# Kernel tuning notes

Hardware: AMD Instinct MI355X
Metric: run time of the kernel (lower is better)

## Reference

```python
import jax, jax.numpy as jnp
import numpy as np

B, H, S, DK = 4, 16, 2048, 128

def setup_inputs() -> dict:
    key = jax.random.key(0)
    kq, kk, kv, km = jax.random.split(key, 4)
    query = jax.random.normal(kq, (B, H, S, DK), dtype=jnp.float32)
    key_t = jax.random.normal(kk, (B, H, S, DK), dtype=jnp.float32)
    value = jax.random.normal(kv, (B, H, S, DK), dtype=jnp.float32)
    mask = jax.random.randint(km, (B, H, S, S), 0, 2, dtype=jnp.int32)
    return {"query": query, "key": key_t, "value": value, "mask": mask}

def reference(query, key, value, mask):
    d_k = query.shape[-1]
    # scores: (b, h, sq, sk)
    scores = jnp.einsum("bhqd,bhkd->bhqk", query, key) / jnp.sqrt(jnp.float32(d_k))
    scores = jnp.where(mask == 0, -jnp.inf, scores)
    weights = jax.nn.softmax(scores, axis=-1)  # dropout p=0.0 -> identity
    out = jnp.einsum("bhqk,bhkd->bhqd", weights, value)
    return out, weights
```

## Files before the change

### kernel.cpp

```cpp
#include <hip/hip_runtime.h>


constexpr int Sc = 2048, Dc = 128;
constexpr int BHc = 64;
constexpr long OUTE = (long)BHc * Sc * Dc;
constexpr long KVE  = (long)BHc * Sc * Dc;
constexpr int QBR = 128;
constexpr int NQT = Sc / QBR;
constexpr int NBLK = BHc * NQT;
#define SCALEF 0.088388347648318447f

typedef __attribute__((ext_vector_type(4))) float f32x4;
typedef _Float16 f16x8 __attribute__((ext_vector_type(8)));

static __device__ __forceinline__ f16x8 loadcvt8h(const float* __restrict__ p) {
  float4 a = *(const float4*)p;
  float4 b = *(const float4*)(p + 4);
  f16x8 r;
  r[0] = (_Float16)a.x; r[1] = (_Float16)a.y; r[2] = (_Float16)a.z; r[3] = (_Float16)a.w;
  r[4] = (_Float16)b.x; r[5] = (_Float16)b.y; r[6] = (_Float16)b.z; r[7] = (_Float16)b.w;
  return r;
}

__global__ __launch_bounds__(256)
void kconv_kernel(const float* __restrict__ K, _Float16* __restrict__ Kh) {
  long i = ((long)blockIdx.x * 256 + threadIdx.x) * 8;
  f16x8 v = loadcvt8h(K + i);
  *(f16x8*)(Kh + i) = v;
}

__global__ __launch_bounds__(256)
void vtrans_kernel(const float* __restrict__ V, _Float16* __restrict__ Vt) {
  __shared__ _Float16 sT[Dc][64 + 2];
  const int bh = blockIdx.x >> 5;
  const int kt = blockIdx.x & 31;
  const int tid = threadIdx.x;
  const float* vb = V + ((long)bh * Sc + kt * 64) * Dc;
  #pragma unroll
  for (int i = 0; i < 8; i++) {
    int e = tid + i * 256;
    int ki = e >> 5;
    int dq = (e & 31) * 4;
    float4 f = *(const float4*)(vb + (long)ki * Dc + dq);
    sT[dq + 0][ki] = (_Float16)f.x;
    sT[dq + 1][ki] = (_Float16)f.y;
    sT[dq + 2][ki] = (_Float16)f.z;
    sT[dq + 3][ki] = (_Float16)f.w;
  }
  __syncthreads();
  #pragma unroll
  for (int i = 0; i < 4; i++) {
    int chunk = tid + i * 256;
    int d = chunk >> 3;
    int kc = (chunk & 7) * 8;
    f16x8 o;
    #pragma unroll
    for (int j = 0; j < 8; j++) o[j] = sT[d][kc + j];
    *(f16x8*)(Vt + ((long)bh * Dc + d) * Sc + kt * 64 + kc) = o;
  }
}

__global__ __launch_bounds__(512, 4)
void sdpa_main(const float* __restrict__ Qg, const int* __restrict__ Mg,
               float* __restrict__ Og, const _Float16* __restrict__ Kh,
               const _Float16* __restrict__ Vt, unsigned* __restrict__ msk) {
  __shared__ __align__(16) _Float16 sKd[2][64][136];
  __shared__ __align__(16) _Float16 sV[128][72];
  __shared__ __align__(16) _Float16 sPw[8][16][76];
  __shared__ float sRinv[QBR];

  const int bid0 = blockIdx.x;
  const int bid  = (bid0 & 7) * (NBLK >> 3) + (bid0 >> 3);
  const int bh = bid >> 4;
  const int qt = bid & (NQT - 1);

  const int tid  = threadIdx.x;
  const int lane = tid & 63;
  const int w = tid >> 6;
  const int g = lane >> 4;
  const int c = lane & 15;

  f16x8 aq[4];
  {
    const float* qp = Qg + ((long)bh * Sc + (long)qt * QBR + w * 16 + c) * Dc + g * 8;
    #pragma unroll
    for (int ch = 0; ch < 4; ch++) aq[ch] = loadcvt8h(qp + ch * 32);
  }

  const _Float16* Kplane = Kh + (long)bh * Sc * Dc;
  const _Float16* Vplane = Vt + (long)bh * Dc * Sc;
  const int* Mwave = Mg + ((long)bh * Sc + (long)qt * QBR + w * 16 + g * 4) * Sc;
  unsigned* mskB = msk + (long)bid0 * (16 * 512);

  const int kr0 = tid >> 4, kd0 = tid & 15;
  const int vr0 = tid >> 3, vc0 = tid & 7;

  auto loadK = [&](int cc, f16x8& a, f16x8& b) {
    a = *(const f16x8*)(Kplane + (long)(cc * 64 + kr0) * Dc + kd0 * 8);
    b = *(const f16x8*)(Kplane + (long)(cc * 64 + kr0 + 32) * Dc + kd0 * 8);
  };
  auto stageK = [&](int p, const f16x8& a, const f16x8& b) {
    *(f16x8*)&sKd[p][kr0][kd0 * 8] = a;
    *(f16x8*)&sKd[p][kr0 + 32][kd0 * 8] = b;
  };
  auto loadV = [&](int cc, f16x8& a, f16x8& b) {
    a = *(const f16x8*)(Vplane + (long)vr0 * Sc + cc * 64 + vc0 * 8);
    b = *(const f16x8*)(Vplane + (long)(vr0 + 64) * Sc + cc * 64 + vc0 * 8);
  };
  auto stageV = [&](const f16x8& a, const f16x8& b) {
    *(f16x8*)&sV[vr0][vc0 * 8] = a;
    *(f16x8*)&sV[vr0 + 64][vc0 * 8] = b;
  };
  auto loadM = [&](int (*dst)[4], int cc) {
    const int* mp = Mwave + cc * 64 + c;
    #pragma unroll
    for (int nt = 0; nt < 4; nt++)
      #pragma unroll
      for (int r = 0; r < 4; r++)
        dst[nt][r] = mp[(long)r * Sc + nt * 16];
  };
  auto packbits = [&](const int (*mv)[4]) -> unsigned {
    unsigned bits = 0;
    #pragma unroll
    for (int nt = 0; nt < 4; nt++)
      #pragma unroll
      for (int r = 0; r < 4; r++)
        bits |= (mv[nt][r] != 0 ? 1u : 0u) << (nt * 4 + r);
    return bits;
  };

  auto qkTile = [&](int p, int nt) -> f32x4 {
    const _Float16* kb = &sKd[p][nt * 16 + c][g * 8];
    f16x8 b0 = *(const f16x8*)kb;
    f16x8 b1 = *(const f16x8*)(kb + 32);
    f16x8 b2 = *(const f16x8*)(kb + 64);
    f16x8 b3 = *(const f16x8*)(kb + 96);
    f32x4 s = {0.f, 0.f, 0.f, 0.f};
    s = __builtin_amdgcn_mfma_f32_16x16x32_f16(aq[0], b0, s, 0, 0, 0);
    s = __builtin_amdgcn_mfma_f32_16x16x32_f16(aq[1], b1, s, 0, 0, 0);
    s = __builtin_amdgcn_mfma_f32_16x16x32_f16(aq[2], b2, s, 0, 0, 0);
    s = __builtin_amdgcn_mfma_f32_16x16x32_f16(aq[3], b3, s, 0, 0, 0);
    return s;
  };

  float rs[4] = {0.f, 0.f, 0.f, 0.f};
  {
    f16x8 ka0, kb0, ka1, kb1;
    int mv0[4][4], mv1[4][4];
    auto bodyA = [&](int p, unsigned bits) {
      #pragma unroll
      for (int nt = 0; nt < 4; nt++) {
        f32x4 s = qkTile(p, nt);
        #pragma unroll
        for (int r = 0; r < 4; r++) {
          float e = ((bits >> (nt * 4 + r)) & 1u) ? __expf(s[r] * SCALEF) : 0.f;
          rs[r] += (float)(_Float16)e;
        }
      }
    };
    loadK(0, ka0, kb0);
    loadM(mv0, 0);
    for (int cc = 0; cc < 32; cc += 2) {
      stageK(0, ka0, kb0);
      __syncthreads();
      loadK(cc + 1, ka1, kb1);
      loadM(mv1, cc + 1);
      const unsigned bits0 = packbits(mv0);
      bodyA(0, bits0);
      stageK(1, ka1, kb1);
      __syncthreads();
      if (cc + 2 < 32) {
        loadK(cc + 2, ka0, kb0);
        loadM(mv0, cc + 2);
      }
      const unsigned bits1 = packbits(mv1);
      mskB[((cc >> 1) << 9) + tid] = bits0 | (bits1 << 16);
      bodyA(1, bits1);
    }
  }
  #pragma unroll
  for (int r = 0; r < 4; r++) {
    float x = rs[r];
    x += __shfl_xor(x, 1);
    x += __shfl_xor(x, 2);
    x += __shfl_xor(x, 4);
    x += __shfl_xor(x, 8);
    if (c == 0) sRinv[w * 16 + g * 4 + r] = (x > 0.f) ? (1.f / x) : 0.f;
  }
  __syncthreads();
  const float rinvW = sRinv[w * 16 + (lane >> 2)];
  float rinvO[4];
  #pragma unroll
  for (int r = 0; r < 4; r++) rinvO[r] = sRinv[w * 16 + g * 4 + r];

  f32x4 oacc[8];
  #pragma unroll
  for (int dt = 0; dt < 8; dt++) oacc[dt] = (f32x4){0.f, 0.f, 0.f, 0.f};
  float* wbase = Og + OUTE + ((long)bh * Sc + (long)qt * QBR + w * 16) * Sc;
  const int wr = lane >> 2;
  const int wq = lane & 3;

  {
    f16x8 ka, kb2, va, vb2;
    loadK(0, ka, kb2);
    loadV(0, va, vb2);
    unsigned bp = mskB[tid];
    unsigned bpn = 0;
    for (int cc = 0; cc < 32; cc++) {
      __syncthreads();
      stageK(0, ka, kb2);
      stageV(va, vb2);
      __syncthreads();
      if (cc + 1 < 32) {
        loadK(cc + 1, ka, kb2);
        loadV(cc + 1, va, vb2);
      }
      if ((cc & 1) == 0 && (cc >> 1) + 1 < 16)
        bpn = mskB[(((cc >> 1) + 1) << 9) + tid];
      const unsigned bits = (cc & 1) ? (bp >> 16) : (bp & 0xffffu);
      #pragma unroll
      for (int nt = 0; nt < 4; nt++) {
        f32x4 s = qkTile(0, nt);
        #pragma unroll
        for (int r = 0; r < 4; r++) {
          float e = ((bits >> (nt * 4 + r)) & 1u) ? __expf(s[r] * SCALEF) : 0.f;
          sPw[w][g * 4 + r][nt * 16 + c] = (_Float16)e;
        }
      }
      {
        f16x8 p0 = *(const f16x8*)&sPw[w][wr][wq * 16];
        f16x8 p1 = *(const f16x8*)&sPw[w][wr][wq * 16 + 8];
        float* dst = wbase + (long)wr * Sc + cc * 64 + wq * 16;
        float4 o0, o1, o2, o3;
        o0.x = (float)p0[0] * rinvW; o0.y = (float)p0[1] * rinvW;
        o0.z = (float)p0[2] * rinvW; o0.w = (float)p0[3] * rinvW;
        o1.x = (float)p0[4] * rinvW; o1.y = (float)p0[5] * rinvW;
        o1.z = (float)p0[6] * rinvW; o1.w = (float)p0[7] * rinvW;
        o2.x = (float)p1[0] * rinvW; o2.y = (float)p1[1] * rinvW;
        o2.z = (float)p1[2] * rinvW; o2.w = (float)p1[3] * rinvW;
        o3.x = (float)p1[4] * rinvW; o3.y = (float)p1[5] * rinvW;
        o3.z = (float)p1[6] * rinvW; o3.w = (float)p1[7] * rinvW;
        *(float4*)dst = o0;
        *(float4*)(dst + 4) = o1;
        *(float4*)(dst + 8) = o2;
        *(float4*)(dst + 12) = o3;
      }
      f16x8 pa0 = *(const f16x8*)&sPw[w][c][g * 8];
      f16x8 pa1 = *(const f16x8*)&sPw[w][c][32 + g * 8];
      #pragma unroll
      for (int dt = 0; dt < 8; dt++) {
        const _Float16* vb = &sV[dt * 16 + c][g * 8];
        f16x8 v0 = *(const f16x8*)vb;
        f16x8 v1 = *(const f16x8*)(vb + 32);
        oacc[dt] = __builtin_amdgcn_mfma_f32_16x16x32_f16(pa0, v0, oacc[dt], 0, 0, 0);
        oacc[dt] = __builtin_amdgcn_mfma_f32_16x16x32_f16(pa1, v1, oacc[dt], 0, 0, 0);
      }
      if (cc & 1) bp = bpn;
    }
  }

  float* ob = Og + ((long)bh * Sc + (long)qt * QBR + w * 16 + g * 4) * Dc;
  #pragma unroll
  for (int r = 0; r < 4; r++) {
    #pragma unroll
    for (int dt = 0; dt < 8; dt++) {
      ob[(long)r * Dc + dt * 16 + c] = oacc[dt][r] * rinvO[r];
    }
  }
}

__global__ __launch_bounds__(256)
void sdpa_naive(const float* __restrict__ Qg, const float* __restrict__ Kg,
                const float* __restrict__ Vg, const int* __restrict__ Mg,
                float* __restrict__ Og) {
  __shared__ float sE[4][Sc];
  const int bh = blockIdx.x >> 9;
  const int rg = blockIdx.x & 511;
  const int wv = threadIdx.x >> 6, ln = threadIdx.x & 63;
  const int qrow = rg * 4 + wv;
  const float* qp = Qg + ((long)bh * Sc + qrow) * Dc;
  const int* mp = Mg + ((long)bh * Sc + qrow) * Sc;
  float rsum = 0.f;
  for (int k0 = 0; k0 < Sc; k0 += 64) {
    const int kcol = k0 + ln;
    const float* kp = Kg + ((long)bh * Sc + kcol) * Dc;
    float s = 0.f;
    for (int d = 0; d < Dc; d++) s += qp[d] * kp[d];
    float e = (mp[kcol] != 0) ? __expf(s * SCALEF) : 0.f;
    e = (float)(_Float16)e;
    sE[wv][kcol] = e;
    rsum += e;
  }
  for (int o = 1; o < 64; o <<= 1) rsum += __shfl_xor(rsum, o);
  float oa = 0.f, ob2 = 0.f;
  for (int k = 0; k < Sc; k++) {
    const float e = sE[wv][k];
    const float* vp = Vg + ((long)bh * Sc + k) * Dc;
    oa += e * vp[ln];
    ob2 += e * vp[ln + 64];
  }
  const float ri = (rsum > 0.f) ? 1.f / rsum : 0.f;
  float* op = Og + ((long)bh * Sc + qrow) * Dc;
  op[ln] = oa * ri;
  op[ln + 64] = ob2 * ri;
  float* wb = Og + OUTE + ((long)bh * Sc + qrow) * Sc;
  for (int k = ln; k < Sc; k += 64) wb[k] = sE[wv][k] * ri;
}

extern "C" void kernel_launch(void* const* d_in, const int* in_sizes, int n_in,
                              void* d_out, int out_size, void* d_ws, size_t ws_size,
                              hipStream_t stream) {
  (void)in_sizes; (void)n_in; (void)out_size;
  const float* q = (const float*)d_in[0];
  const float* k = (const float*)d_in[1];
  const float* v = (const float*)d_in[2];
  const int* m = (const int*)d_in[3];
  float* out = (float*)d_out;

  const size_t need = 2UL * KVE * sizeof(_Float16) + (size_t)NBLK * 16 * 512 * 4;
  if (d_ws != nullptr && ws_size >= need) {
    _Float16* Kh = (_Float16*)d_ws;
    _Float16* Vt = Kh + KVE;
    unsigned* msk = (unsigned*)(Vt + KVE);
    hipLaunchKernelGGL(kconv_kernel, dim3((int)(KVE / 8 / 256)), dim3(256), 0, stream, k, Kh);
    hipLaunchKernelGGL(vtrans_kernel, dim3(BHc * 32), dim3(256), 0, stream, v, Vt);
    hipLaunchKernelGGL(sdpa_main, dim3(NBLK), dim3(512), 0, stream, q, m, out, Kh, Vt, msk);
  } else {
    hipLaunchKernelGGL(sdpa_naive, dim3(BHc * 512), dim3(256), 0, stream, q, k, v, m, out);
  }
}
```

Measured before the change: 704.9 us.

## Double-buffer K tiles in LDS and read V directly from global memory

Drops the shared-memory staging of V. Each wave now loads its V fragments straight from global memory inside the PV MFMA loop. K gets a two-stage LDS double buffer, and the main loop is unrolled by two so there is one barrier per chunk instead of two. The K row padding changes from 136 to 138 halves. This removes V's LDS traffic and halves the barriers, but each of the 8 waves now re-reads the same V chunk through the caches. The new row stride also breaks 16-byte alignment of the vector LDS writes.

```diff
diff --git a/kernel.cpp b/kernel.cpp
--- a/kernel.cpp
+++ b/kernel.cpp
@@ -64,8 +64,7 @@
 void sdpa_main(const float* __restrict__ Qg, const int* __restrict__ Mg,
                float* __restrict__ Og, const _Float16* __restrict__ Kh,
                const _Float16* __restrict__ Vt, unsigned* __restrict__ msk) {
-  __shared__ __align__(16) _Float16 sKd[2][64][136];
-  __shared__ __align__(16) _Float16 sV[128][72];
+  __shared__ __align__(16) _Float16 sKd[2][64][138];
   __shared__ __align__(16) _Float16 sPw[8][16][76];
   __shared__ float sRinv[QBR];
 
@@ -93,7 +92,6 @@
   unsigned* mskB = msk + (long)bid0 * (16 * 512);
 
   const int kr0 = tid >> 4, kd0 = tid & 15;
-  const int vr0 = tid >> 3, vc0 = tid & 7;
 
   auto loadK = [&](int cc, f16x8& a, f16x8& b) {
     a = *(const f16x8*)(Kplane + (long)(cc * 64 + kr0) * Dc + kd0 * 8);
@@ -102,14 +100,6 @@
   auto stageK = [&](int p, const f16x8& a, const f16x8& b) {
     *(f16x8*)&sKd[p][kr0][kd0 * 8] = a;
     *(f16x8*)&sKd[p][kr0 + 32][kd0 * 8] = b;
-  };
-  auto loadV = [&](int cc, f16x8& a, f16x8& b) {
-    a = *(const f16x8*)(Vplane + (long)vr0 * Sc + cc * 64 + vc0 * 8);
-    b = *(const f16x8*)(Vplane + (long)(vr0 + 64) * Sc + cc * 64 + vc0 * 8);
-  };
-  auto stageV = [&](const f16x8& a, const f16x8& b) {
-    *(f16x8*)&sV[vr0][vc0 * 8] = a;
-    *(f16x8*)&sV[vr0 + 64][vc0 * 8] = b;
   };
   auto loadM = [&](int (*dst)[4], int cc) {
     const int* mp = Mwave + cc * 64 + c;
@@ -201,26 +191,10 @@
   const int wq = lane & 3;
 
   {
-    f16x8 ka, kb2, va, vb2;
-    loadK(0, ka, kb2);
-    loadV(0, va, vb2);
-    unsigned bp = mskB[tid];
-    unsigned bpn = 0;
-    for (int cc = 0; cc < 32; cc++) {
-      __syncthreads();
-      stageK(0, ka, kb2);
-      stageV(va, vb2);
-      __syncthreads();
-      if (cc + 1 < 32) {
-        loadK(cc + 1, ka, kb2);
-        loadV(cc + 1, va, vb2);
-      }
-      if ((cc & 1) == 0 && (cc >> 1) + 1 < 16)
-        bpn = mskB[(((cc >> 1) + 1) << 9) + tid];
-      const unsigned bits = (cc & 1) ? (bp >> 16) : (bp & 0xffffu);
+    auto bodyB = [&](int p, int cc, unsigned bits) {
       #pragma unroll
       for (int nt = 0; nt < 4; nt++) {
-        f32x4 s = qkTile(0, nt);
+        f32x4 s = qkTile(p, nt);
         #pragma unroll
         for (int r = 0; r < 4; r++) {
           float e = ((bits >> (nt * 4 + r)) & 1u) ? __expf(s[r] * SCALEF) : 0.f;
@@ -249,13 +223,35 @@
       f16x8 pa1 = *(const f16x8*)&sPw[w][c][32 + g * 8];
       #pragma unroll
       for (int dt = 0; dt < 8; dt++) {
-        const _Float16* vb = &sV[dt * 16 + c][g * 8];
-        f16x8 v0 = *(const f16x8*)vb;
-        f16x8 v1 = *(const f16x8*)(vb + 32);
+        const _Float16* vp = Vplane + (long)(dt * 16 + c) * Sc + cc * 64 + g * 8;
+        f16x8 v0 = *(const f16x8*)vp;
+        f16x8 v1 = *(const f16x8*)(vp + 32);
         oacc[dt] = __builtin_amdgcn_mfma_f32_16x16x32_f16(pa0, v0, oacc[dt], 0, 0, 0);
         oacc[dt] = __builtin_amdgcn_mfma_f32_16x16x32_f16(pa1, v1, oacc[dt], 0, 0, 0);
       }
-      if (cc & 1) bp = bpn;
+    };
+
+    f16x8 k0a, k0b, k1a, k1b;
+    unsigned bp, bpn = 0;
+    bp = mskB[tid];
+    loadK(0, k0a, k0b);
+    __syncthreads();
+    stageK(0, k0a, k0b);
+    loadK(1, k1a, k1b);
+    __syncthreads();
+    for (int cc = 0; cc < 32; cc += 2) {
+      if (cc + 2 < 32) loadK(cc + 2, k0a, k0b);
+      if ((cc >> 1) + 1 < 16) bpn = mskB[(((cc >> 1) + 1) << 9) + tid];
+      bodyB(0, cc, bp & 0xffffu);
+      stageK(1, k1a, k1b);
+      __syncthreads();
+      if (cc + 3 < 32) loadK(cc + 3, k1a, k1b);
+      bodyB(1, cc + 1, bp >> 16);
+      if (cc + 2 < 32) {
+        stageK(0, k0a, k0b);
+        __syncthreads();
+      }
+      bp = bpn;
     }
   }
 
```

Measured after the change: 1.314 ms. +86.4%, slower.
